# Performance work log

Hardware: AMD Instinct MI355X
Metric: run time of the kernel (lower is better)

Reference implementation:

```python
import jax, jax.numpy as jnp
import numpy as np

ACT_BITS = 8
W_BITS = 8
C_IN = 64


def round_ste(x):
    # straight-through rounding (Brevitas training behavior)
    return x + jax.lax.stop_gradient(jnp.round(x) - x)


def fake_quant(x, scale, bits, signed):
    if signed:
        lo, hi = -(2 ** (bits - 1)), 2 ** (bits - 1) - 1
    else:
        lo, hi = 0, 2 ** bits - 1
    return jnp.clip(round_ste(x / scale), lo, hi) * scale


def conv_nchw(x, w, pad, groups=1):
    return jax.lax.conv_general_dilated(
        x, w, window_strides=(1, 1), padding=((pad, pad), (pad, pad)),
        dimension_numbers=("NCHW", "OIHW", "NCHW"), feature_group_count=groups)


def setup_inputs() -> dict:
    key = jax.random.key(0)
    k0, k1, k2, k3 = jax.random.split(key, 4)
    x = jax.random.normal(k0, (8, 64, 112, 112), jnp.float32)
    w1 = jax.random.normal(k1, (64, 1, 3, 3), jnp.float32) * 0.05    # depthwise 3x3
    w2 = jax.random.normal(k2, (128, 64, 1, 1), jnp.float32) * 0.05  # pointwise 1x1
    w_sc = jax.random.normal(k3, (128, 64, 1, 1), jnp.float32) * 0.05  # shortcut 1x1
    sc = lambda v: jnp.asarray(v, jnp.float32)
    return dict(x=x, w1=w1, w2=w2, w_sc=w_sc,
                s_in=sc(0.03), s_relu=sc(0.02), s_add=sc(0.03),
                sw1=sc(0.004), sw2=sc(0.004), sw_sc=sc(0.004))


def reference(x, w1, w2, w_sc, s_in, s_relu, s_add, sw1, sw2, sw_sc):
    # quant_input: signed 8-bit fake-quant of the activation
    xq = fake_quant(x, s_in, ACT_BITS, True)
    # shortcut: 1x1 conv with int8 fake-quantized weights (inplane != ouplane)
    identity = conv_nchw(xq, fake_quant(w_sc, sw_sc, W_BITS, True), pad=0)
    # conv1: depthwise 3x3 (groups=inplane) with int8 fake-quantized weights
    y = conv_nchw(xq, fake_quant(w1, sw1, W_BITS, True), pad=1, groups=C_IN)
    # relu2: QuantReLU -> unsigned 8-bit fake-quant of relu
    y = fake_quant(jax.nn.relu(y), s_relu, ACT_BITS, False)
    # conv2: pointwise 1x1
    y = conv_nchw(y, fake_quant(w2, sw2, W_BITS, True), pad=0)
    # residual_add: add then requantize to signed 8-bit
    return fake_quant(y + identity, s_add, ACT_BITS, True)
```

## Files before the change

kernel.cpp:

```cpp
#include <hip/hip_runtime.h>
#include <hip/hip_bf16.h>
#include <stdint.h>

#define NIMG 8
#define CIN  64
#define HWI  12544
#define COUT 128

typedef short v8s __attribute__((ext_vector_type(8)));
typedef float v4f __attribute__((ext_vector_type(4)));

static __device__ __forceinline__ int q8(float x, float inv, float lo, float hi) {
    float t = rintf(x * inv);
    t = fminf(fmaxf(t, lo), hi);
    return (int)t;
}

static __device__ __forceinline__ uint32_t funnel(uint32_t hi, uint32_t lo, int sh) {
    return (uint32_t)(((((uint64_t)hi) << 32) | (uint64_t)lo) >> sh);
}

static __device__ __forceinline__ int dot4(uint32_t a, uint32_t b, int c) {
    int acc = c;
    #pragma unroll
    for (int i = 0; i < 4; ++i)
        acc += (int)(int8_t)(a >> (8*i)) * (int)(int8_t)(b >> (8*i));
    return acc;
}

static __device__ __forceinline__ uint16_t i2bf(int v) {
    union { float f; uint32_t u; } c; c.f = (float)v;
    return (uint16_t)(c.u >> 16);
}

__global__ void __launch_bounds__(256) wprep_kernel(
    const float* __restrict__ w2, const float* __restrict__ wsc,
    const float* __restrict__ sw2p, const float* __restrict__ swscp,
    uint16_t* __restrict__ wbuf)
{
    int t = blockIdx.x * 256 + threadIdx.x;
    int f = t * 4;
    int co = f >> 6, k = f & 63;
    float inv2 = 1.0f / sw2p[0];
    float invs = 1.0f / swscp[0];
    float4 a = *(const float4*)(w2 + f);
    float4 b = *(const float4*)(wsc + f);
    float av[4] = {a.x, a.y, a.z, a.w};
    float bv[4] = {b.x, b.y, b.z, b.w};
    uint16_t* d2 = wbuf + co*128 + k;
    uint16_t* ds = wbuf + co*128 + 64 + k;
    *(ushort2*)(d2)     = make_ushort2(i2bf(q8(av[0], inv2, -128.f, 127.f)),
                                       i2bf(q8(av[1], inv2, -128.f, 127.f)));
    *(ushort2*)(d2 + 2) = make_ushort2(i2bf(q8(av[2], inv2, -128.f, 127.f)),
                                       i2bf(q8(av[3], inv2, -128.f, 127.f)));
    *(ushort2*)(ds)     = make_ushort2(i2bf(q8(bv[0], invs, -128.f, 127.f)),
                                       i2bf(q8(bv[1], invs, -128.f, 127.f)));
    *(ushort2*)(ds + 2) = make_ushort2(i2bf(q8(bv[2], invs, -128.f, 127.f)),
                                       i2bf(q8(bv[3], invs, -128.f, 127.f)));
}

__global__ void __launch_bounds__(256, 4) fused_kernel(
    const float* __restrict__ x, const float* __restrict__ w1,
    const uint16_t* __restrict__ wbuf,
    const float* __restrict__ sinp, const float* __restrict__ srelup,
    const float* __restrict__ saddp, const float* __restrict__ sw1p,
    const float* __restrict__ sw2p, const float* __restrict__ swscp,
    float* __restrict__ out)
{
    __shared__ int8_t tile[64 * 348];
    __shared__ int8_t Bl[112 * 132];

    int bid = blockIdx.x;
    int n = bid / 112, h = bid - n*112;
    int tid = threadIdx.x;
    int wave = tid >> 6, lane = tid & 63;
    int lr = lane >> 4, ln = lane & 15;
    float sin_f = sinp[0];
    float inv_sin = 1.0f / sin_f;

    int c = lane;
    float isw1 = 1.0f / sw1p[0];
    uint32_t wp[3];
    #pragma unroll
    for (int ky = 0; ky < 3; ++ky) {
        uint32_t pk = 0;
        #pragma unroll
        for (int kx = 0; kx < 3; ++kx) {
            int q = q8(w1[c*9 + ky*3 + kx], isw1, -128.0f, 127.0f);
            pk |= (uint32_t)(q & 255) << (8*kx);
        }
        wp[ky] = pk;
    }

    v8s a[2][4];
    #pragma unroll
    for (int mi = 0; mi < 2; ++mi) {
        int m = (wave*2 + mi)*16 + ln;
        #pragma unroll
        for (int seg = 0; seg < 4; ++seg)
            a[mi][seg] = *(const v8s*)(wbuf + (size_t)m*128 + seg*32 + lr*8);
    }

    #pragma unroll
    for (int b = 0; b < 3; ++b) {
        float4 vals[7];
        #pragma unroll
        for (int i = 0; i < 7; ++i) {
            int id = tid + (b*7 + i)*256;
            int cc = id / 84; int rem = id - cc*84;
            int r = rem / 28; int seg = rem - r*28;
            int grow = h + r - 1;
            vals[i] = make_float4(0.f, 0.f, 0.f, 0.f);
            if ((unsigned)grow < 112u)
                vals[i] = *(const float4*)(x + ((size_t)(n*64 + cc) * HWI + grow*112 + seg*4));
        }
        #pragma unroll
        for (int i = 0; i < 7; ++i) {
            int id = tid + (b*7 + i)*256;
            int cc = id / 84; int rem = id - cc*84;
            int r = rem / 28; int seg = rem - r*28;
            float vv[4] = {vals[i].x, vals[i].y, vals[i].z, vals[i].w};
            uint32_t pk = 0;
            #pragma unroll
            for (int e = 0; e < 4; ++e) {
                int q = q8(vv[e], inv_sin, -128.0f, 127.0f);
                pk |= (uint32_t)(q & 255) << (8*e);
            }
            *(uint32_t*)&tile[cc*348 + r*116 + seg*4] = pk;
        }
    }
    if (tid < 192) {
        int cc = tid / 3, r = tid - cc*3;
        *(uint32_t*)&tile[cc*348 + r*116 + 112] = 0;
    }
    __syncthreads();

    {
        int w0b = wave * 28;
        float r1 = (sin_f * sw1p[0]) / srelup[0];

        int base[3];
        #pragma unroll
        for (int r2 = 0; r2 < 3; ++r2) base[r2] = c*348 + r2*116;

        uint32_t Ar[3], Br[3], Cr[3];
        #pragma unroll
        for (int r2 = 0; r2 < 3; ++r2) {
            Ar[r2] = wave ? *(uint32_t*)&tile[base[r2] + w0b - 4] : 0u;
            Br[r2] = *(uint32_t*)&tile[base[r2] + w0b];
            Cr[r2] = *(uint32_t*)&tile[base[r2] + w0b + 4];
        }

        #pragma unroll
        for (int q = 0; q < 7; ++q) {
            int acc0 = 0, acc1 = 0, acc2 = 0, acc3 = 0;
            #pragma unroll
            for (int r2 = 0; r2 < 3; ++r2) {
                uint32_t d0 = funnel(Br[r2], Ar[r2], 24);
                uint32_t d1 = Br[r2];
                uint32_t d2 = funnel(Cr[r2], Br[r2], 8);
                uint32_t d3 = funnel(Cr[r2], Br[r2], 16);
                acc0 = dot4(d0, wp[r2], acc0);
                acc1 = dot4(d1, wp[r2], acc1);
                acc2 = dot4(d2, wp[r2], acc2);
                acc3 = dot4(d3, wp[r2], acc3);
            }
            int accs[4] = {acc0, acc1, acc2, acc3};
            uint32_t xdw = Br[1];
            int pxb = w0b + q*4;
            #pragma unroll
            for (int j = 0; j < 4; ++j) {
                float t = rintf((float)accs[j] * r1);
                t = fminf(fmaxf(t, 0.0f), 255.0f);
                Bl[(pxb + j)*132 + c]      = (int8_t)(int)t;
                Bl[(pxb + j)*132 + 64 + c] = (int8_t)((xdw >> (8*j)) & 255);
            }
            #pragma unroll
            for (int r2 = 0; r2 < 3; ++r2) { Ar[r2] = Br[r2]; Br[r2] = Cr[r2]; }
            if (q < 6) {
                #pragma unroll
                for (int r2 = 0; r2 < 3; ++r2)
                    Cr[r2] = *(uint32_t*)&tile[base[r2] + w0b + q*4 + 8];
            }
        }
    }
    __syncthreads();

    {
        float S2  = sw2p[0] * srelup[0];
        float Ssc = swscp[0] * sinp[0];
        float sadd = saddp[0];
        float inv_sadd = 1.0f / sadd;

        size_t orow = (size_t)n*COUT*HWI + (size_t)h*112;

        for (int nt = 0; nt < 7; ++nt) {
            int boff = (nt*16 + ln)*132 + lr*8;
            v8s bf[4];
            #pragma unroll
            for (int seg = 0; seg < 4; ++seg) {
                uint32_t d0 = *(const uint32_t*)&Bl[boff + seg*32];
                uint32_t d1 = *(const uint32_t*)&Bl[boff + seg*32 + 4];
                v8s t;
                if (seg < 2) {
                    #pragma unroll
                    for (int e = 0; e < 4; ++e) {
                        t[e]     = (short)i2bf((int)((d0 >> (8*e)) & 255u));
                        t[4 + e] = (short)i2bf((int)((d1 >> (8*e)) & 255u));
                    }
                } else {
                    #pragma unroll
                    for (int e = 0; e < 4; ++e) {
                        t[e]     = (short)i2bf((int)(int8_t)(d0 >> (8*e)));
                        t[4 + e] = (short)i2bf((int)(int8_t)(d1 >> (8*e)));
                    }
                }
                bf[seg] = t;
            }
            #pragma unroll
            for (int mi = 0; mi < 2; ++mi) {
                v4f acc2 = {0.f, 0.f, 0.f, 0.f};
                v4f accs = {0.f, 0.f, 0.f, 0.f};
                acc2 = __builtin_amdgcn_mfma_f32_16x16x32_bf16(a[mi][0], bf[0], acc2, 0, 0, 0);
                acc2 = __builtin_amdgcn_mfma_f32_16x16x32_bf16(a[mi][1], bf[1], acc2, 0, 0, 0);
                accs = __builtin_amdgcn_mfma_f32_16x16x32_bf16(a[mi][2], bf[2], accs, 0, 0, 0);
                accs = __builtin_amdgcn_mfma_f32_16x16x32_bf16(a[mi][3], bf[3], accs, 0, 0, 0);
                size_t obase = orow + (size_t)((wave*2 + mi)*16 + lr*4)*HWI + nt*16 + ln;
                #pragma unroll
                for (int r = 0; r < 4; ++r) {
                    float v = S2 * acc2[r] + Ssc * accs[r];
                    float t = rintf(v * inv_sadd);
                    t = fminf(fmaxf(t, -128.0f), 127.0f);
                    out[obase + (size_t)r*HWI] = t * sadd;
                }
            }
        }
    }
}

extern "C" void kernel_launch(void* const* d_in, const int* in_sizes, int n_in,
                              void* d_out, int out_size, void* d_ws, size_t ws_size,
                              hipStream_t stream) {
    const float* x     = (const float*)d_in[0];
    const float* w1    = (const float*)d_in[1];
    const float* w2    = (const float*)d_in[2];
    const float* wsc   = (const float*)d_in[3];
    const float* sin   = (const float*)d_in[4];
    const float* srelu = (const float*)d_in[5];
    const float* sadd  = (const float*)d_in[6];
    const float* sw1   = (const float*)d_in[7];
    const float* sw2   = (const float*)d_in[8];
    const float* swsc  = (const float*)d_in[9];

    uint16_t* wbuf = (uint16_t*)d_ws;

    wprep_kernel<<<8, 256, 0, stream>>>(w2, wsc, sw2, swsc, wbuf);
    fused_kernel<<<NIMG * 112, 256, 0, stream>>>(x, w1, wbuf,
                                                 sin, srelu, sadd, sw1, sw2, swsc,
                                                 (float*)d_out);
}
```

Measured before the change: 118.7 us.

## Switch pointwise and shortcut GEMMs from bf16 MFMA to int8 MFMA with offset correction

```diff
diff --git a/kernel.cpp b/kernel.cpp
--- a/kernel.cpp
+++ b/kernel.cpp
@@ -7,8 +7,7 @@
 #define HWI  12544
 #define COUT 128
 
-typedef short v8s __attribute__((ext_vector_type(8)));
-typedef float v4f __attribute__((ext_vector_type(4)));
+typedef int v4i __attribute__((ext_vector_type(4)));
 
 static __device__ __forceinline__ int q8(float x, float inv, float lo, float hi) {
     float t = rintf(x * inv);
@@ -21,22 +20,21 @@
 }
 
 static __device__ __forceinline__ int dot4(uint32_t a, uint32_t b, int c) {
+#if __has_builtin(__builtin_amdgcn_sdot4)
+    return __builtin_amdgcn_sdot4((int)a, (int)b, c, false);
+#else
     int acc = c;
     #pragma unroll
     for (int i = 0; i < 4; ++i)
         acc += (int)(int8_t)(a >> (8*i)) * (int)(int8_t)(b >> (8*i));
     return acc;
-}
-
-static __device__ __forceinline__ uint16_t i2bf(int v) {
-    union { float f; uint32_t u; } c; c.f = (float)v;
-    return (uint16_t)(c.u >> 16);
+#endif
 }
 
 __global__ void __launch_bounds__(256) wprep_kernel(
     const float* __restrict__ w2, const float* __restrict__ wsc,
     const float* __restrict__ sw2p, const float* __restrict__ swscp,
-    uint16_t* __restrict__ wbuf)
+    int8_t* __restrict__ wbuf, int* __restrict__ offs)
 {
     int t = blockIdx.x * 256 + threadIdx.x;
     int f = t * 4;
@@ -47,28 +45,35 @@
     float4 b = *(const float4*)(wsc + f);
     float av[4] = {a.x, a.y, a.z, a.w};
     float bv[4] = {b.x, b.y, b.z, b.w};
-    uint16_t* d2 = wbuf + co*128 + k;
-    uint16_t* ds = wbuf + co*128 + 64 + k;
-    *(ushort2*)(d2)     = make_ushort2(i2bf(q8(av[0], inv2, -128.f, 127.f)),
-                                       i2bf(q8(av[1], inv2, -128.f, 127.f)));
-    *(ushort2*)(d2 + 2) = make_ushort2(i2bf(q8(av[2], inv2, -128.f, 127.f)),
-                                       i2bf(q8(av[3], inv2, -128.f, 127.f)));
-    *(ushort2*)(ds)     = make_ushort2(i2bf(q8(bv[0], invs, -128.f, 127.f)),
-                                       i2bf(q8(bv[1], invs, -128.f, 127.f)));
-    *(ushort2*)(ds + 2) = make_ushort2(i2bf(q8(bv[2], invs, -128.f, 127.f)),
-                                       i2bf(q8(bv[3], invs, -128.f, 127.f)));
+    uint32_t pa = 0, pb = 0;
+    int partial = 0;
+    #pragma unroll
+    for (int j = 0; j < 4; ++j) {
+        int qa = q8(av[j], inv2, -128.f, 127.f);
+        int qb = q8(bv[j], invs, -128.f, 127.f);
+        partial += qa;
+        pa |= (uint32_t)(qa & 255) << (8*j);
+        pb |= (uint32_t)(qb & 255) << (8*j);
+    }
+    *(uint32_t*)(wbuf + co*128 + k)      = pa;
+    *(uint32_t*)(wbuf + co*128 + 64 + k) = pb;
+    partial += __shfl_xor(partial, 1, 16);
+    partial += __shfl_xor(partial, 2, 16);
+    partial += __shfl_xor(partial, 4, 16);
+    partial += __shfl_xor(partial, 8, 16);
+    if ((t & 15) == 0) offs[co] = partial << 7;
 }
 
 __global__ void __launch_bounds__(256, 4) fused_kernel(
     const float* __restrict__ x, const float* __restrict__ w1,
-    const uint16_t* __restrict__ wbuf,
+    const int8_t* __restrict__ wbuf, const int* __restrict__ offs,
     const float* __restrict__ sinp, const float* __restrict__ srelup,
     const float* __restrict__ saddp, const float* __restrict__ sw1p,
     const float* __restrict__ sw2p, const float* __restrict__ swscp,
     float* __restrict__ out)
 {
     __shared__ int8_t tile[64 * 348];
-    __shared__ int8_t Bl[112 * 132];
+    __shared__ int8_t Bl[112 * 144];
 
     int bid = blockIdx.x;
     int n = bid / 112, h = bid - n*112;
@@ -92,13 +97,15 @@
         wp[ky] = pk;
     }
 
-    v8s a[2][4];
+    v4i a[2][2];
+    int4 ofr[2];
     #pragma unroll
     for (int mi = 0; mi < 2; ++mi) {
-        int m = (wave*2 + mi)*16 + ln;
-        #pragma unroll
-        for (int seg = 0; seg < 4; ++seg)
-            a[mi][seg] = *(const v8s*)(wbuf + (size_t)m*128 + seg*32 + lr*8);
+        int mt = wave*2 + mi;
+        int m = mt*16 + ln;
+        a[mi][0] = *(const v4i*)(wbuf + (size_t)m*128 + lr*16);
+        a[mi][1] = *(const v4i*)(wbuf + (size_t)m*128 + 64 + lr*16);
+        ofr[mi]  = *(const int4*)(offs + mt*16 + lr*4);
     }
 
     #pragma unroll
@@ -172,8 +179,8 @@
             for (int j = 0; j < 4; ++j) {
                 float t = rintf((float)accs[j] * r1);
                 t = fminf(fmaxf(t, 0.0f), 255.0f);
-                Bl[(pxb + j)*132 + c]      = (int8_t)(int)t;
-                Bl[(pxb + j)*132 + 64 + c] = (int8_t)((xdw >> (8*j)) & 255);
+                Bl[(pxb + j)*144 + c]      = (int8_t)((int)t - 128);
+                Bl[(pxb + j)*144 + 64 + c] = (int8_t)((xdw >> (8*j)) & 255);
             }
             #pragma unroll
             for (int r2 = 0; r2 < 3; ++r2) { Ar[r2] = Br[r2]; Br[r2] = Cr[r2]; }
@@ -195,40 +202,20 @@
         size_t orow = (size_t)n*COUT*HWI + (size_t)h*112;
 
         for (int nt = 0; nt < 7; ++nt) {
-            int boff = (nt*16 + ln)*132 + lr*8;
-            v8s bf[4];
-            #pragma unroll
-            for (int seg = 0; seg < 4; ++seg) {
-                uint32_t d0 = *(const uint32_t*)&Bl[boff + seg*32];
-                uint32_t d1 = *(const uint32_t*)&Bl[boff + seg*32 + 4];
-                v8s t;
-                if (seg < 2) {
-                    #pragma unroll
-                    for (int e = 0; e < 4; ++e) {
-                        t[e]     = (short)i2bf((int)((d0 >> (8*e)) & 255u));
-                        t[4 + e] = (short)i2bf((int)((d1 >> (8*e)) & 255u));
-                    }
-                } else {
-                    #pragma unroll
-                    for (int e = 0; e < 4; ++e) {
-                        t[e]     = (short)i2bf((int)(int8_t)(d0 >> (8*e)));
-                        t[4 + e] = (short)i2bf((int)(int8_t)(d1 >> (8*e)));
-                    }
-                }
-                bf[seg] = t;
-            }
+            int px = nt*16 + ln;
+            const int8_t* bp = &Bl[px*144 + lr*16];
+            v4i b0 = *(const v4i*)bp;
+            v4i b1 = *(const v4i*)(bp + 64);
             #pragma unroll
             for (int mi = 0; mi < 2; ++mi) {
-                v4f acc2 = {0.f, 0.f, 0.f, 0.f};
-                v4f accs = {0.f, 0.f, 0.f, 0.f};
-                acc2 = __builtin_amdgcn_mfma_f32_16x16x32_bf16(a[mi][0], bf[0], acc2, 0, 0, 0);
-                acc2 = __builtin_amdgcn_mfma_f32_16x16x32_bf16(a[mi][1], bf[1], acc2, 0, 0, 0);
-                accs = __builtin_amdgcn_mfma_f32_16x16x32_bf16(a[mi][2], bf[2], accs, 0, 0, 0);
-                accs = __builtin_amdgcn_mfma_f32_16x16x32_bf16(a[mi][3], bf[3], accs, 0, 0, 0);
-                size_t obase = orow + (size_t)((wave*2 + mi)*16 + lr*4)*HWI + nt*16 + ln;
+                v4i z = {0, 0, 0, 0};
+                v4i c2 = __builtin_amdgcn_mfma_i32_16x16x64_i8(a[mi][0], b0, z, 0, 0, 0);
+                v4i cs = __builtin_amdgcn_mfma_i32_16x16x64_i8(a[mi][1], b1, z, 0, 0, 0);
+                int o4[4] = {ofr[mi].x, ofr[mi].y, ofr[mi].z, ofr[mi].w};
+                size_t obase = orow + (size_t)((wave*2 + mi)*16 + lr*4)*HWI + px;
                 #pragma unroll
                 for (int r = 0; r < 4; ++r) {
-                    float v = S2 * acc2[r] + Ssc * accs[r];
+                    float v = S2 * (float)(c2[r] + o4[r]) + Ssc * (float)cs[r];
                     float t = rintf(v * inv_sadd);
                     t = fminf(fmaxf(t, -128.0f), 127.0f);
                     out[obase + (size_t)r*HWI] = t * sadd;
@@ -252,10 +239,11 @@
     const float* sw2   = (const float*)d_in[8];
     const float* swsc  = (const float*)d_in[9];
 
-    uint16_t* wbuf = (uint16_t*)d_ws;
-
-    wprep_kernel<<<8, 256, 0, stream>>>(w2, wsc, sw2, swsc, wbuf);
-    fused_kernel<<<NIMG * 112, 256, 0, stream>>>(x, w1, wbuf,
+    int8_t* wbuf = (int8_t*)d_ws;
+    int*    offs = (int*)(wbuf + (size_t)COUT * 128);
+
+    wprep_kernel<<<8, 256, 0, stream>>>(w2, wsc, sw2, swsc, wbuf, offs);
+    fused_kernel<<<NIMG * 112, 256, 0, stream>>>(x, w1, wbuf, offs,
                                                  sin, srelu, sadd, sw1, sw2, swsc,
                                                  (float*)d_out);
 }
```

New measurement: 116.6 us. Within noise of the previous version (-1.8%).
